# Performance work log

Hardware: AMD Instinct MI355X
Metric: run time of the kernel (lower is better)

Reference implementation:

```python
import jax, jax.numpy as jnp
import numpy as np

EMBEDDING_SIZE = 50
MAX_DOCUMENT_LENGTH = 100
MAX_LABEL = 15
VOCAB = 200000
HID = 1024
BATCH = 4096


def setup_inputs() -> dict:
    key = jax.random.key(0)
    ks = jax.random.split(key, 8)
    x = jax.random.randint(ks[0], (BATCH, MAX_DOCUMENT_LENGTH), 0, VOCAB)
    emb_table = jax.random.normal(ks[1], (VOCAB, EMBEDDING_SIZE), jnp.float32) * 0.05
    # Keras GRUCell (reset_after=True): kernel [E,3H], recurrent_kernel [H,3H],
    # bias [2,3H] split into input bias and recurrent bias; gate order z, r, h.
    kernel = jax.random.normal(ks[2], (EMBEDDING_SIZE, 3 * HID), jnp.float32) * (1.0 / np.sqrt(EMBEDDING_SIZE))
    rec_kernel = jax.random.normal(ks[3], (HID, 3 * HID), jnp.float32) * (1.0 / np.sqrt(HID))
    bias_i = jnp.zeros((3 * HID,), jnp.float32)
    bias_r = jnp.zeros((3 * HID,), jnp.float32)
    Wd = jax.random.normal(ks[4], (HID, MAX_LABEL), jnp.float32) * (1.0 / np.sqrt(HID))
    bd = jnp.zeros((MAX_LABEL,), jnp.float32)
    return {"x": x, "drop_rate": 0, "emb_table": emb_table, "kernel": kernel,
            "rec_kernel": rec_kernel, "bias_i": bias_i, "bias_r": bias_r,
            "Wd": Wd, "bd": bd}


def _gru_scan(emb, kernel, rec_kernel, bias_i, bias_r):
    # emb: [B,T,E] -> time-major [T,B,E]
    emb_t = jnp.transpose(emb, (1, 0, 2))
    B = emb.shape[0]
    h0 = jnp.zeros((B, HID), emb.dtype)

    def step(h, x_t):
        xp = x_t @ kernel + bias_i            # [B,3H]
        hp = h @ rec_kernel + bias_r          # [B,3H]
        xz, xr, xh = jnp.split(xp, 3, axis=-1)
        hz, hr, hh = jnp.split(hp, 3, axis=-1)
        z = jax.nn.sigmoid(xz + hz)
        r = jax.nn.sigmoid(xr + hr)
        hcand = jnp.tanh(xh + r * hh)
        h_new = z * h + (1.0 - z) * hcand
        return h_new, None

    h_last, _ = jax.lax.scan(step, h0, emb_t)
    return h_last


def reference(x, drop_rate, emb_table, kernel, rec_kernel, bias_i, bias_r, Wd, bd):
    emb = emb_table[x]                         # [B,T,E]
    encoding = _gru_scan(emb, kernel, rec_kernel, bias_i, bias_r)  # [B,H]
    if drop_rate > 0:                          # drop_rate is a static Python int
        keep = 1.0 - float(drop_rate)
        mask = jax.random.bernoulli(jax.random.key(1), keep, encoding.shape)
        encoding = jnp.where(mask, encoding / keep, 0.0)
    logits = encoding @ Wd + bd                # [B,15]
    return logits
```

## Files before the change

kernel.cpp:

```cpp
#include <hip/hip_runtime.h>
#include <stdint.h>

#define H_DIM   1024
#define G3      3072
#define EMB     50
#define TSTEPS  100
#define NB      4096
#define NLABEL  15

typedef __bf16 bf16x8 __attribute__((ext_vector_type(8)));
typedef float  f32x4  __attribute__((ext_vector_type(4)));

__device__ inline uint16_t f2bf(float f) {
  uint32_t u = __builtin_bit_cast(uint32_t, f);
  u += 0x7FFFu + ((u >> 16) & 1u);
  return (uint16_t)(u >> 16);
}

__device__ inline void gld16(const void* g, void* l) {
  __builtin_amdgcn_global_load_lds(
      (const __attribute__((address_space(1))) uint32_t*)g,
      (__attribute__((address_space(3))) uint32_t*)l, 16, 0, 0);
}

#define BARF() do { __builtin_amdgcn_s_barrier(); \
                    asm volatile("" ::: "memory"); } while (0)


__global__ __launch_bounds__(256) void prep_recT(const float* __restrict__ rec,
                                                 uint16_t* __restrict__ recT) {
  __shared__ uint16_t st[64][72];
  const int n0 = blockIdx.x * 64;
  const int k0 = blockIdx.y * 64;
  const int tid = threadIdx.x;
#pragma unroll
  for (int i = 0; i < 16; ++i) {
    int idx = tid + i * 256;
    int r = idx >> 6;
    int c = idx & 63;
    st[c][r] = f2bf(rec[(size_t)(k0 + r) * G3 + n0 + c]);
  }
  __syncthreads();
#pragma unroll
  for (int i = 0; i < 16; ++i) {
    int idx = tid + i * 256;
    int r = idx >> 6;
    int c = idx & 63;
    recT[(size_t)(n0 + r) * H_DIM + k0 + c] = st[r][c];
  }
}

__global__ __launch_bounds__(256) void prep_kerT(const float* __restrict__ ker,
                                                 uint16_t* __restrict__ kerT) {
  int n = blockIdx.x * 4 + (threadIdx.x >> 6);
  int k = threadIdx.x & 63;
  float v = (k < EMB) ? ker[(size_t)k * G3 + n] : 0.f;
  kerT[(size_t)n * 64 + k] = f2bf(v);
}

__global__ __launch_bounds__(256) void prep_embt(const int* __restrict__ x,
                                                 const float* __restrict__ tab,
                                                 uint16_t* __restrict__ embt) {
  int idx = blockIdx.x * 256 + threadIdx.x;
  int g = idx >> 5;
  int p = idx & 31;
  int t = g >> 12;
  int b = g & 4095;
  int row = x[b * TSTEPS + t];
  float2 v;
  if (p < 25) v = *reinterpret_cast<const float2*>(tab + (size_t)row * EMB + 2 * p);
  else { v.x = 0.f; v.y = 0.f; }
  uint32_t packed = (uint32_t)f2bf(v.x) | ((uint32_t)f2bf(v.y) << 16);
  *reinterpret_cast<uint32_t*>(embt + (size_t)g * 64 + 2 * p) = packed;
}

__global__ __launch_bounds__(256, 2) void gru_step_kernel(
    const uint16_t* __restrict__ hb_prev,
    float* __restrict__ hf,
    uint16_t* __restrict__ hb_next,
    const uint16_t* __restrict__ recT,
    const uint16_t* __restrict__ kerT,
    const uint16_t* __restrict__ embt,
    const float* __restrict__ bias_i,
    const float* __restrict__ bias_r) {
  __shared__ __align__(16) uint16_t sA2[2][128 * 64];
  __shared__ __align__(16) uint16_t sP[2][3][64 * 64];

  const int tid  = threadIdx.x;
  const int lane = tid & 63;
  const int wid  = tid >> 6;
  const int wm   = wid >> 1;
  const int wn   = wid & 1;
  const int bid  = blockIdx.x;
  const int xk = bid & 7, slot = bid >> 3;
  const int rowblk = (xk >> 1) * 8 + (slot >> 3);
  const int colblk = (xk & 1) * 8 + (slot & 7);
  const int r0 = rowblk * 128;
  const int j0 = colblk * 64;

  const int swz8 = 8 * ((lane & 7) ^ (lane >> 3));

  bf16x8 af[4][2];
  bf16x8 bf0[2][2], bf1[2][2];
  f32x4 accZ[4][2], accR[4][2], accH[4][2], accX[4][2];
#pragma unroll
  for (int m = 0; m < 4; ++m)
#pragma unroll
    for (int n = 0; n < 2; ++n) {
      accZ[m][n] = (f32x4){0.f, 0.f, 0.f, 0.f};
      accR[m][n] = (f32x4){0.f, 0.f, 0.f, 0.f};
      accH[m][n] = (f32x4){0.f, 0.f, 0.f, 0.f};
      accX[m][n] = (f32x4){0.f, 0.f, 0.f, 0.f};
    }

  auto stageA = [&](int t) {
    const int abuf = t & 1;
#pragma unroll
    for (int i = 0; i < 4; ++i) {
      int chunk = wid * 4 + i;
      int row = chunk * 8 + (lane >> 3);
      const uint16_t* src = (t < 16)
          ? hb_prev + (size_t)(r0 + row) * H_DIM + t * 64 + swz8
          : embt + (size_t)(r0 + row) * 64 + swz8;
      gld16(src, &sA2[abuf][(chunk * 64 + lane) * 8]);
    }
  };
  auto stageP = [&](int t, int g) {
    const int pbuf = t & 1;
#pragma unroll
    for (int i = 0; i < 2; ++i) {
      int c = wid * 2 + i;
      int n = c * 8 + (lane >> 3);
      const uint16_t* src = (t < 16)
          ? recT + ((size_t)g * H_DIM + j0 + n) * H_DIM + t * 64 + swz8
          : kerT + ((size_t)g * H_DIM + j0 + n) * 64 + swz8;
      gld16(src, &sP[pbuf][g][(c * 64 + lane) * 8]);
    }
  };
  auto readA = [&](int t) {
    const int abuf = t & 1;
#pragma unroll
    for (int ks = 0; ks < 2; ++ks) {
      const int colswz = (ks * 32 + (lane >> 4) * 8) ^ ((lane & 7) << 3);
#pragma unroll
      for (int mf = 0; mf < 4; ++mf)
        af[mf][ks] = *reinterpret_cast<const bf16x8*>(
            &sA2[abuf][(wm * 64 + mf * 16 + (lane & 15)) * 64 + colswz]);
    }
  };
  auto readB = [&](int t, int g, bf16x8 (&bf)[2][2]) {
    const int pbuf = t & 1;
#pragma unroll
    for (int ks = 0; ks < 2; ++ks) {
      const int colswz = (ks * 32 + (lane >> 4) * 8) ^ ((lane & 7) << 3);
#pragma unroll
      for (int nf = 0; nf < 2; ++nf) {
        int nn = wn * 32 + nf * 16 + (lane & 15);
        bf[nf][ks] = *reinterpret_cast<const bf16x8*>(&sP[pbuf][g][nn * 64 + colswz]);
      }
    }
  };
  auto MF = [&](bf16x8 (&bf)[2][2], f32x4 (&acc)[4][2]) {
    __builtin_amdgcn_s_setprio(1);
#pragma unroll
    for (int ks = 0; ks < 2; ++ks)
#pragma unroll
      for (int nf = 0; nf < 2; ++nf)
#pragma unroll
        for (int mf = 0; mf < 4; ++mf)
          acc[mf][nf] = __builtin_amdgcn_mfma_f32_16x16x32_bf16(
              af[mf][ks], bf[nf][ks], acc[mf][nf], 0, 0, 0);
    __builtin_amdgcn_s_setprio(0);
  };

#define PH(DSRD, MFBUF, MFACC, STG, WN) do { \
    DSRD; MF(MFBUF, MFACC); STG; \
    asm volatile("s_waitcnt vmcnt(" #WN ")" ::: "memory"); \
    BARF(); \
  } while (0)
#define PHH(MFBUF, MFACC, DSRD, STG, WN) do { \
    MF(MFBUF, MFACC); DSRD; STG; \
    asm volatile("s_waitcnt vmcnt(" #WN ")" ::: "memory"); \
    BARF(); \
  } while (0)
#define TILE_STEADY(t, BFA, BFB) do { \
    PH(readB(t, 1, BFB), BFA, accZ, stageP((t) + 1, 1), 8); \
    PH(readB(t, 2, BFA), BFB, accR, stageP((t) + 1, 2), 4); \
    PHH(BFA, accH, (readA((t) + 1), readB((t) + 1, 0, BFB)), \
        (stageA((t) + 2), stageP((t) + 2, 0)), 8); \
  } while (0)

  stageA(0); stageP(0, 0); stageP(0, 1); stageP(0, 2);
  stageA(1); stageP(1, 0);
  asm volatile("s_waitcnt vmcnt(0)" ::: "memory");
  BARF();
  readA(0); readB(0, 0, bf0);

  for (int tt = 0; tt < 14; tt += 2) {
    TILE_STEADY(tt, bf0, bf1);
    TILE_STEADY(tt + 1, bf1, bf0);
  }
  TILE_STEADY(14, bf0, bf1);
  PH(readB(15, 1, bf0), bf1, accZ, stageP(16, 1), 8);
  PH(readB(15, 2, bf1), bf0, accR, stageP(16, 2), 4);
  PHH(bf1, accH, (readA(16), readB(16, 0, bf0)), (void)0, 2);
  PH(readB(16, 1, bf1), bf0, accZ, (void)0, 0);
  PH(readB(16, 2, bf0), bf1, accR, (void)0, 0);
  MF(bf0, accX);

#undef PH
#undef PHH
#undef TILE_STEADY

#pragma unroll
  for (int nf = 0; nf < 2; ++nf) {
    int col = j0 + wn * 32 + nf * 16 + (lane & 15);
    float b_z = bias_i[col] + bias_r[col];
    float b_r = bias_i[H_DIM + col] + bias_r[H_DIM + col];
    float bih = bias_i[2 * H_DIM + col];
    float brh = bias_r[2 * H_DIM + col];
#pragma unroll
    for (int mf = 0; mf < 4; ++mf) {
#pragma unroll
      for (int q = 0; q < 4; ++q) {
        int row = r0 + wm * 64 + mf * 16 + (lane >> 4) * 4 + q;
        float z  = 1.f / (1.f + __expf(-(accZ[mf][nf][q] + b_z)));
        float rr = 1.f / (1.f + __expf(-(accR[mf][nf][q] + b_r)));
        float pre = accX[mf][nf][q] + bih + rr * (accH[mf][nf][q] + brh);
        float hc  = 2.f / (1.f + __expf(-2.f * pre)) - 1.f;
        size_t idx = (size_t)row * H_DIM + col;
        float hold = hf[idx];
        float hnew = z * hold + (1.f - z) * hc;
        hf[idx] = hnew;
        hb_next[idx] = f2bf(hnew);
      }
    }
  }
}

__global__ __launch_bounds__(64) void logits_kernel(const float* __restrict__ hf,
                                                    const float* __restrict__ Wd,
                                                    const float* __restrict__ bd,
                                                    float* __restrict__ out) {
  int b = blockIdx.x;
  int l = threadIdx.x;
  float p[NLABEL];
#pragma unroll
  for (int o = 0; o < NLABEL; ++o) p[o] = 0.f;
  for (int kb = 0; kb < 16; ++kb) {
    int k = kb * 64 + l;
    float hv = hf[(size_t)b * H_DIM + k];
#pragma unroll
    for (int o = 0; o < NLABEL; ++o) p[o] += hv * Wd[k * NLABEL + o];
  }
#pragma unroll
  for (int o = 0; o < NLABEL; ++o) {
#pragma unroll
    for (int s = 32; s; s >>= 1) p[o] += __shfl_xor(p[o], s);
  }
  if (l == 0) {
#pragma unroll
    for (int o = 0; o < NLABEL; ++o) out[(size_t)b * NLABEL + o] = p[o] + bd[o];
  }
}

extern "C" void kernel_launch(void* const* d_in, const int* in_sizes, int n_in,
                              void* d_out, int out_size, void* d_ws, size_t ws_size,
                              hipStream_t stream) {
  const int*   x          = (const int*)d_in[0];
  const float* emb_table  = (const float*)d_in[2];
  const float* kernel_w   = (const float*)d_in[3];
  const float* rec_kernel = (const float*)d_in[4];
  const float* bias_i     = (const float*)d_in[5];
  const float* bias_r     = (const float*)d_in[6];
  const float* Wd         = (const float*)d_in[7];
  const float* bd         = (const float*)d_in[8];
  float* out = (float*)d_out;

  char* ws = (char*)d_ws;
  size_t off = 0;
  auto alloc = [&](size_t bytes) {
    char* p = ws + off;
    off += (bytes + 255) & ~(size_t)255;
    return p;
  };
  float*    hf   = (float*)alloc((size_t)NB * H_DIM * 4);
  uint16_t* hb0  = (uint16_t*)alloc((size_t)NB * H_DIM * 2);
  uint16_t* hb1  = (uint16_t*)alloc((size_t)NB * H_DIM * 2);
  uint16_t* recT = (uint16_t*)alloc((size_t)G3 * H_DIM * 2);
  uint16_t* kerT = (uint16_t*)alloc((size_t)G3 * 64 * 2);
  uint16_t* embt = (uint16_t*)alloc((size_t)TSTEPS * NB * 64 * 2);
  if (off > ws_size) return;

  hipMemsetAsync(hf, 0, (size_t)NB * H_DIM * 4, stream);
  hipMemsetAsync(hb0, 0, (size_t)NB * H_DIM * 2, stream);

  prep_recT<<<dim3(G3 / 64, H_DIM / 64), 256, 0, stream>>>(rec_kernel, recT);
  prep_kerT<<<G3 / 4, 256, 0, stream>>>(kernel_w, kerT);
  prep_embt<<<TSTEPS * NB * 32 / 256, 256, 0, stream>>>(x, emb_table, embt);

  uint16_t* hb[2] = {hb0, hb1};
  for (int t = 0; t < TSTEPS; ++t) {
    gru_step_kernel<<<512, 256, 0, stream>>>(
        hb[t & 1], hf, hb[(t + 1) & 1], recT, kerT,
        embt + (size_t)t * NB * 64, bias_i, bias_r);
  }
  logits_kernel<<<NB, 64, 0, stream>>>(hf, Wd, bd, out);
}
```

Baseline: 3.504 ms.

## Load recurrent weight fragments directly from global into registers, bypassing LDS

The weight (B) operands for the three gates are no longer staged through shared memory. Each lane now issues global_load_dwordx4 straight into MFMA operand registers, with a three-gate register pipeline and explicit vmcnt waits, leaving only the A operand (h and embeddings) double-buffered in LDS. This cuts LDS traffic and removes two of the three barriers per k-tile. In exchange it adds register pressure, relies on hand-counted waitcnt ordering, and loses LDS-level reuse of weights across waves (wm pairs now load the same B data twice from global/L2).

```diff
diff --git a/kernel.cpp b/kernel.cpp
--- a/kernel.cpp
+++ b/kernel.cpp
@@ -10,6 +10,7 @@
 
 typedef __bf16 bf16x8 __attribute__((ext_vector_type(8)));
 typedef float  f32x4  __attribute__((ext_vector_type(4)));
+typedef int    i32x4  __attribute__((ext_vector_type(4)));
 
 __device__ inline uint16_t f2bf(float f) {
   uint32_t u = __builtin_bit_cast(uint32_t, f);
@@ -23,8 +24,15 @@
       (__attribute__((address_space(3))) uint32_t*)l, 16, 0, 0);
 }
 
+#define VM(n) do { asm volatile("s_waitcnt vmcnt(" #n ")" ::: "memory"); \
+                   __builtin_amdgcn_sched_barrier(0); } while (0)
+#define LGKM0() do { asm volatile("s_waitcnt lgkmcnt(0)" ::: "memory"); \
+                     __builtin_amdgcn_sched_barrier(0); } while (0)
 #define BARF() do { __builtin_amdgcn_s_barrier(); \
                     asm volatile("" ::: "memory"); } while (0)
+#define GLDB(dst, addr, OFF) \
+  asm volatile("global_load_dwordx4 %0, %1, off offset:" OFF \
+               : "=&v"(dst) : "v"(addr) : "memory")
 
 
 __global__ __launch_bounds__(256) void prep_recT(const float* __restrict__ rec,
@@ -84,7 +92,6 @@
     const float* __restrict__ bias_i,
     const float* __restrict__ bias_r) {
   __shared__ __align__(16) uint16_t sA2[2][128 * 64];
-  __shared__ __align__(16) uint16_t sP[2][3][64 * 64];
 
   const int tid  = threadIdx.x;
   const int lane = tid & 63;
@@ -101,7 +108,7 @@
   const int swz8 = 8 * ((lane & 7) ^ (lane >> 3));
 
   bf16x8 af[4][2];
-  bf16x8 bf0[2][2], bf1[2][2];
+  i32x4  bfv[3][2][2];
   f32x4 accZ[4][2], accR[4][2], accH[4][2], accX[4][2];
 #pragma unroll
   for (int m = 0; m < 4; ++m)
@@ -112,6 +119,15 @@
       accH[m][n] = (f32x4){0.f, 0.f, 0.f, 0.f};
       accX[m][n] = (f32x4){0.f, 0.f, 0.f, 0.f};
     }
+
+  const uint16_t* bB[3][2];
+#pragma unroll
+  for (int g = 0; g < 3; ++g)
+#pragma unroll
+    for (int nf = 0; nf < 2; ++nf)
+      bB[g][nf] = recT +
+          (size_t)(g * H_DIM + j0 + wn * 32 + nf * 16 + (lane & 15)) * H_DIM +
+          (lane >> 4) * 8;
 
   auto stageA = [&](int t) {
     const int abuf = t & 1;
@@ -125,18 +141,6 @@
       gld16(src, &sA2[abuf][(chunk * 64 + lane) * 8]);
     }
   };
-  auto stageP = [&](int t, int g) {
-    const int pbuf = t & 1;
-#pragma unroll
-    for (int i = 0; i < 2; ++i) {
-      int c = wid * 2 + i;
-      int n = c * 8 + (lane >> 3);
-      const uint16_t* src = (t < 16)
-          ? recT + ((size_t)g * H_DIM + j0 + n) * H_DIM + t * 64 + swz8
-          : kerT + ((size_t)g * H_DIM + j0 + n) * 64 + swz8;
-      gld16(src, &sP[pbuf][g][(c * 64 + lane) * 8]);
-    }
-  };
   auto readA = [&](int t) {
     const int abuf = t & 1;
 #pragma unroll
@@ -148,69 +152,69 @@
             &sA2[abuf][(wm * 64 + mf * 16 + (lane & 15)) * 64 + colswz]);
     }
   };
-  auto readB = [&](int t, int g, bf16x8 (&bf)[2][2]) {
-    const int pbuf = t & 1;
-#pragma unroll
-    for (int ks = 0; ks < 2; ++ks) {
-      const int colswz = (ks * 32 + (lane >> 4) * 8) ^ ((lane & 7) << 3);
-#pragma unroll
-      for (int nf = 0; nf < 2; ++nf) {
-        int nn = wn * 32 + nf * 16 + (lane & 15);
-        bf[nf][ks] = *reinterpret_cast<const bf16x8*>(&sP[pbuf][g][nn * 64 + colswz]);
-      }
-    }
-  };
-  auto MF = [&](bf16x8 (&bf)[2][2], f32x4 (&acc)[4][2]) {
-    __builtin_amdgcn_s_setprio(1);
-#pragma unroll
-    for (int ks = 0; ks < 2; ++ks)
+
+#define ISSUE_BG(g, P0, P1) do { \
+    GLDB(bfv[g][0][0], P0, "0");  GLDB(bfv[g][0][1], P0, "64"); \
+    GLDB(bfv[g][1][0], P1, "0");  GLDB(bfv[g][1][1], P1, "64"); \
+  } while (0)
+#define MFG(g, ACC) do { \
+    __builtin_amdgcn_s_setprio(1); \
+    _Pragma("unroll") for (int ks = 0; ks < 2; ++ks) \
+    _Pragma("unroll") for (int nf = 0; nf < 2; ++nf) \
+    _Pragma("unroll") for (int mf = 0; mf < 4; ++mf) \
+      ACC[mf][nf] = __builtin_amdgcn_mfma_f32_16x16x32_bf16( \
+          af[mf][ks], __builtin_bit_cast(bf16x8, bfv[g][nf][ks]), \
+          ACC[mf][nf], 0, 0, 0); \
+    __builtin_amdgcn_s_setprio(0); \
+  } while (0)
+
+  stageA(0); stageA(1);
+  ISSUE_BG(0, bB[0][0], bB[0][1]);
+  ISSUE_BG(1, bB[1][0], bB[1][1]);
+  ISSUE_BG(2, bB[2][0], bB[2][1]);
+#pragma unroll
+  for (int g = 0; g < 3; ++g) { bB[g][0] += 64; bB[g][1] += 64; }
+  VM(12);
+  BARF();
+  readA(0);
+
+  for (int t = 0; t < 15; ++t) {
+    stageA(t + 2);
+    VM(12);
+    MFG(0, accZ); ISSUE_BG(0, bB[0][0], bB[0][1]);
+    VM(12);
+    MFG(1, accR); ISSUE_BG(1, bB[1][0], bB[1][1]);
+    VM(12);
+    MFG(2, accH); ISSUE_BG(2, bB[2][0], bB[2][1]);
+#pragma unroll
+    for (int g = 0; g < 3; ++g) { bB[g][0] += 64; bB[g][1] += 64; }
+    readA(t + 1);
+    LGKM0();
+    VM(12);
+    BARF();
+  }
+
+  {
+    const uint16_t* kB[3][2];
+#pragma unroll
+    for (int g = 0; g < 3; ++g)
 #pragma unroll
       for (int nf = 0; nf < 2; ++nf)
-#pragma unroll
-        for (int mf = 0; mf < 4; ++mf)
-          acc[mf][nf] = __builtin_amdgcn_mfma_f32_16x16x32_bf16(
-              af[mf][ks], bf[nf][ks], acc[mf][nf], 0, 0, 0);
-    __builtin_amdgcn_s_setprio(0);
-  };
-
-#define PH(DSRD, MFBUF, MFACC, STG, WN) do { \
-    DSRD; MF(MFBUF, MFACC); STG; \
-    asm volatile("s_waitcnt vmcnt(" #WN ")" ::: "memory"); \
-    BARF(); \
-  } while (0)
-#define PHH(MFBUF, MFACC, DSRD, STG, WN) do { \
-    MF(MFBUF, MFACC); DSRD; STG; \
-    asm volatile("s_waitcnt vmcnt(" #WN ")" ::: "memory"); \
-    BARF(); \
-  } while (0)
-#define TILE_STEADY(t, BFA, BFB) do { \
-    PH(readB(t, 1, BFB), BFA, accZ, stageP((t) + 1, 1), 8); \
-    PH(readB(t, 2, BFA), BFB, accR, stageP((t) + 1, 2), 4); \
-    PHH(BFA, accH, (readA((t) + 1), readB((t) + 1, 0, BFB)), \
-        (stageA((t) + 2), stageP((t) + 2, 0)), 8); \
-  } while (0)
-
-  stageA(0); stageP(0, 0); stageP(0, 1); stageP(0, 2);
-  stageA(1); stageP(1, 0);
-  asm volatile("s_waitcnt vmcnt(0)" ::: "memory");
-  BARF();
-  readA(0); readB(0, 0, bf0);
-
-  for (int tt = 0; tt < 14; tt += 2) {
-    TILE_STEADY(tt, bf0, bf1);
-    TILE_STEADY(tt + 1, bf1, bf0);
-  }
-  TILE_STEADY(14, bf0, bf1);
-  PH(readB(15, 1, bf0), bf1, accZ, stageP(16, 1), 8);
-  PH(readB(15, 2, bf1), bf0, accR, stageP(16, 2), 4);
-  PHH(bf1, accH, (readA(16), readB(16, 0, bf0)), (void)0, 2);
-  PH(readB(16, 1, bf1), bf0, accZ, (void)0, 0);
-  PH(readB(16, 2, bf0), bf1, accR, (void)0, 0);
-  MF(bf0, accX);
-
-#undef PH
-#undef PHH
-#undef TILE_STEADY
+        kB[g][nf] = kerT +
+            (size_t)(g * H_DIM + j0 + wn * 32 + nf * 16 + (lane & 15)) * 64 +
+            (lane >> 4) * 8;
+    VM(8);  MFG(0, accZ); ISSUE_BG(0, kB[0][0], kB[0][1]);
+    VM(8);  MFG(1, accR); ISSUE_BG(1, kB[1][0], kB[1][1]);
+    VM(8);  MFG(2, accH); ISSUE_BG(2, kB[2][0], kB[2][1]);
+    readA(16);
+    LGKM0();
+  }
+  VM(8);  MFG(0, accZ);
+  VM(4);  MFG(1, accR);
+  VM(0);  MFG(2, accX);
+
+#undef ISSUE_BG
+#undef MFG
 
 #pragma unroll
   for (int nf = 0; nf < 2; ++nf) {
```

New measurement: 5.841 ms. +66.7%, slower.
